# Performance work log

Measured on AMD Instinct MI355X. Metric: run time of the kernel, lower is better.

## Reference

```python
import math
import jax, jax.numpy as jnp
import numpy as np

# Constants (module-level in original repo; plausible biological values)
LATENCY_EPSILON = 1e-6
HAIR_CELL_COMPRESSION_EXPONENT = 0.3
HAIR_CELL_ADAPTATION_SUPPRESSION = 0.5
AUDITORY_NERVE_ADAPTATION_DECAY = 0.9
AUDITORY_NERVE_ADAPTATION_RATE = 0.1

SAMPLE_RATE = 16000
N_FFT = 512
N_FILTERS = 128
OUTPUT_SIZE = 262144
N_TIMESTEPS = 128
SPARSITY = 0.05
F_MIN, F_MAX = 80.0, 7600.0


def build_filterbank() -> np.ndarray:
    """Mel triangular filterbank, faithful to _create_filterbank (integer bin edges)."""
    hz_to_mel = lambda hz: 2595.0 * math.log10(1.0 + hz / 700.0)
    mel_to_hz = lambda mel: 700.0 * (10.0 ** (mel / 2595.0) - 1.0)
    mel_pts = np.linspace(hz_to_mel(F_MIN), hz_to_mel(F_MAX), N_FILTERS + 2)
    hz_pts = np.array([mel_to_hz(m) for m in mel_pts])
    bins = (hz_pts * N_FFT / SAMPLE_RATE).astype(np.int64)  # .long() truncation
    fb = np.zeros((N_FILTERS, N_FFT // 2 + 1), dtype=np.float32)
    for i in range(N_FILTERS):
        l, c, r = bins[i], bins[i + 1], bins[i + 2]
        for j in range(l, c):
            if c > l:
                fb[i, j] = (j - l) / (c - l)
        for j in range(c, r):
            if r > c:
                fb[i, j] = (r - j) / (r - c)
    return fb


def setup_inputs() -> dict:
    key = jax.random.key(0)
    k_audio, k_w = jax.random.split(key)
    audio = jax.random.normal(k_audio, (SAMPLE_RATE,), dtype=jnp.float32)
    filterbank = jnp.asarray(build_filterbank())  # [n_filters, n_fft//2+1]
    W = jax.random.normal(k_w, (OUTPUT_SIZE, N_FILTERS), dtype=jnp.float32) * 0.02
    b = jnp.zeros((OUTPUT_SIZE,), dtype=jnp.float32)
    adaptation_state = jnp.zeros((N_FILTERS,), dtype=jnp.float32)
    return {"audio": audio, "filterbank": filterbank, "W": W, "b": b,
            "adaptation_state": adaptation_state}


def reference(audio, filterbank, W, b, adaptation_state):
    # Basilar membrane: rfft with n=N_FFT (truncates audio to first N_FFT samples)
    spec = jnp.fft.rfft(audio, n=N_FFT)            # [n_fft//2+1] complex
    magnitude = jnp.abs(spec).astype(jnp.float32)   # [257]
    cochlear = filterbank @ magnitude               # [n_filters]
    # Hair cell compression
    hair = jnp.power(cochlear + LATENCY_EPSILON, HAIR_CELL_COMPRESSION_EXPONENT)
    adapted = jax.nn.relu(hair - adaptation_state * HAIR_CELL_ADAPTATION_SUPPRESSION)
    # Output projection (torch Linear: x @ W.T + b)
    activity = W @ adapted + b                      # [output_size]
    # Latency coding: high activity -> early spike (vectorized scatter)
    a_min, a_max = activity.min(), activity.max()
    norm = (activity - a_min) / (a_max - a_min + 1e-6)
    latencies = ((1.0 - norm) * (N_TIMESTEPS - 1)).astype(jnp.int32)  # [output_size]
    fire = norm > SPARSITY                           # [output_size]
    # spikes[t, n] = fire[n] and latencies[n] == t
    spikes = (latencies[None, :] == jnp.arange(N_TIMESTEPS, dtype=jnp.int32)[:, None]) \
             & fire[None, :]                         # [n_timesteps, output_size] bool
    return spikes
```

## Files before the change

kernel.cpp:

```cpp
#include <hip/hip_runtime.h>
#include <math.h>

#ifndef M_PI
#define M_PI 3.14159265358979323846
#endif

#define N_FFT       512
#define N_BINS      257
#define N_FILTERS   128
#define OUTPUT_SIZE 262144
#define N_TIMESTEPS 128

__device__ __forceinline__ unsigned long long enc_d(double f) {
    unsigned long long u = (unsigned long long)__double_as_longlong(f);
    return (u & 0x8000000000000000ull) ? ~u : (u | 0x8000000000000000ull);
}
__device__ __forceinline__ double dec_d(unsigned long long e) {
    unsigned long long u = (e & 0x8000000000000000ull) ? (e ^ 0x8000000000000000ull) : ~e;
    return __longlong_as_double((long long)u);
}

__global__ __launch_bounds__(256) void k1_frontend(
    const float* __restrict__ audio, const float* __restrict__ fb,
    const float* __restrict__ adapt, double* __restrict__ adapted,
    unsigned long long* __restrict__ minmax)
{
    __shared__ double tw_c[N_FFT];
    __shared__ double tw_s[N_FFT];
    __shared__ double aud[N_FFT];
    __shared__ float  mag[N_BINS];

    const int tid = threadIdx.x;

    for (int m = tid; m < N_FFT; m += 256) {
        double ang = (-2.0 * M_PI * (double)m) / (double)N_FFT;
        double s, c;
        sincos(ang, &s, &c);
        tw_c[m] = c;
        tw_s[m] = s;
        aud[m] = (double)audio[m];
    }
    __syncthreads();

    for (int b = tid; b < N_BINS; b += 256) {
        double re = 0.0, im = 0.0;
        int m = 0;
        for (int n = 0; n < N_FFT; ++n) {
            double a = aud[n];
            re += a * tw_c[m];
            im += a * tw_s[m];
            m = (m + b) & (N_FFT - 1);
        }
        mag[b] = (float)sqrt(re * re + im * im);
    }
    __syncthreads();

    if (tid < N_FILTERS) {
        double acc = 0.0;
        const float* row = fb + tid * N_BINS;
        for (int j = 0; j < N_BINS; ++j)
            acc += (double)row[j] * (double)mag[j];
        double x = acc + 1e-6;
        double p = pow(x, 0.3);
        double a = p - (double)adapt[tid] * 0.5;
        adapted[tid] = a > 0.0 ? a : 0.0;
    }
    if (tid == 0) {
        minmax[0] = 0xFFFFFFFFFFFFFFFFull;
        minmax[1] = 0ull;
    }
}

__global__ __launch_bounds__(256) void k2_gemv(
    const float4* __restrict__ W4, const float* __restrict__ bias,
    const double* __restrict__ adapted, double* __restrict__ activity,
    unsigned long long* __restrict__ minmax)
{
    __shared__ double ad[N_FILTERS];
    __shared__ double red_min[256];
    __shared__ double red_max[256];

    const int tid = threadIdx.x;
    if (tid < N_FILTERS) ad[tid] = adapted[tid];
    __syncthreads();

    const int row = blockIdx.x * 256 + tid;
    const float4* wrow = W4 + (size_t)row * (N_FILTERS / 4);

    double acc = 0.0;
    #pragma unroll 8
    for (int j = 0; j < N_FILTERS / 4; ++j) {
        float4 w = wrow[j];
        const int k = j * 4;
        acc += (double)w.x * ad[k];
        acc += (double)w.y * ad[k + 1];
        acc += (double)w.z * ad[k + 2];
        acc += (double)w.w * ad[k + 3];
    }
    double a = acc + (double)bias[row];
    activity[row] = a;

    red_min[tid] = a;
    red_max[tid] = a;
    __syncthreads();
    for (int s = 128; s > 0; s >>= 1) {
        if (tid < s) {
            red_min[tid] = fmin(red_min[tid], red_min[tid + s]);
            red_max[tid] = fmax(red_max[tid], red_max[tid + s]);
        }
        __syncthreads();
    }
    if (tid == 0) {
        atomicMin(&minmax[0], enc_d(red_min[0]));
        atomicMax(&minmax[1], enc_d(red_max[0]));
    }
}

__global__ __launch_bounds__(256) void k3_spikes(
    const double* __restrict__ activity,
    const unsigned long long* __restrict__ minmax,
    int4* __restrict__ out4)
{
    const int tid = blockIdx.x * 256 + threadIdx.x;
    const double amin = dec_d(minmax[0]);
    const double amax = dec_d(minmax[1]);
    const double denom = (amax - amin) + 1e-6;

    const double ax = activity[4 * tid + 0];
    const double ay = activity[4 * tid + 1];
    const double az = activity[4 * tid + 2];
    const double aw = activity[4 * tid + 3];

    const double nx = (ax - amin) / denom;
    const double ny = (ay - amin) / denom;
    const double nz = (az - amin) / denom;
    const double nw = (aw - amin) / denom;

    const int lx = (int)((1.0 - nx) * 127.0);
    const int ly = (int)((1.0 - ny) * 127.0);
    const int lz = (int)((1.0 - nz) * 127.0);
    const int lw = (int)((1.0 - nw) * 127.0);

    const int vx = (nx > 0.05) ? 1 : 0;
    const int vy = (ny > 0.05) ? 1 : 0;
    const int vz = (nz > 0.05) ? 1 : 0;
    const int vw = (nw > 0.05) ? 1 : 0;

    #pragma unroll 4
    for (int t = 0; t < N_TIMESTEPS; ++t) {
        int4 v;
        v.x = (lx == t) ? vx : 0;
        v.y = (ly == t) ? vy : 0;
        v.z = (lz == t) ? vz : 0;
        v.w = (lw == t) ? vw : 0;
        out4[(size_t)t * (OUTPUT_SIZE / 4) + tid] = v;
    }
}

extern "C" void kernel_launch(void* const* d_in, const int* in_sizes, int n_in,
                              void* d_out, int out_size, void* d_ws, size_t ws_size,
                              hipStream_t stream) {
    (void)in_sizes; (void)n_in; (void)out_size; (void)ws_size;

    const float* audio = (const float*)d_in[0];
    const float* fb    = (const float*)d_in[1];
    const float* W     = (const float*)d_in[2];
    const float* bias  = (const float*)d_in[3];
    const float* adapt = (const float*)d_in[4];
    int* out = (int*)d_out;

    double* activity = (double*)d_ws;
    double* adapted  = activity + OUTPUT_SIZE;
    unsigned long long* minmax =
        (unsigned long long*)(adapted + N_FILTERS);

    k1_frontend<<<1, 256, 0, stream>>>(audio, fb, adapt, adapted, minmax);
    k2_gemv<<<OUTPUT_SIZE / 256, 256, 0, stream>>>(
        (const float4*)W, bias, adapted, activity, minmax);
    k3_spikes<<<(OUTPUT_SIZE / 4) / 256, 256, 0, stream>>>(
        activity, minmax, (int4*)out);
}
```

Measured before the change: 316.6 us.

## Split DFT bins across two half-sums and spread spike stores over timestep grid

The single-block frontend now runs with 512 threads and has each thread compute half of one DFT bin's sum, then combines the two partials through shared memory. This roughly halves the serial DFT latency on that one block. The spike kernel gains a second grid dimension so each block writes only a quarter of the timesteps, with nontemporal vector stores. That gives more blocks in flight for the 128 MB output write, but each block reloads the activity values and recomputes the normalization four times.

Measured after the change: 341.2 us. 1.08x slower.

```diff
diff --git a/kernel.cpp b/kernel.cpp
--- a/kernel.cpp
+++ b/kernel.cpp
@@ -11,6 +11,8 @@
 #define OUTPUT_SIZE 262144
 #define N_TIMESTEPS 128
 
+typedef int int4v __attribute__((ext_vector_type(4)));
+
 __device__ __forceinline__ unsigned long long enc_d(double f) {
     unsigned long long u = (unsigned long long)__double_as_longlong(f);
     return (u & 0x8000000000000000ull) ? ~u : (u | 0x8000000000000000ull);
@@ -20,7 +22,7 @@
     return __longlong_as_double((long long)u);
 }
 
-__global__ __launch_bounds__(256) void k1_frontend(
+__global__ __launch_bounds__(512) void k1_frontend(
     const float* __restrict__ audio, const float* __restrict__ fb,
     const float* __restrict__ adapt, double* __restrict__ adapted,
     unsigned long long* __restrict__ minmax)
@@ -28,41 +30,55 @@
     __shared__ double tw_c[N_FFT];
     __shared__ double tw_s[N_FFT];
     __shared__ double aud[N_FFT];
+    __shared__ double re_p[2 * N_BINS];
+    __shared__ double im_p[2 * N_BINS];
     __shared__ float  mag[N_BINS];
 
     const int tid = threadIdx.x;
 
-    for (int m = tid; m < N_FFT; m += 256) {
-        double ang = (-2.0 * M_PI * (double)m) / (double)N_FFT;
+    if (tid < N_FFT) {
+        double ang = (-2.0 * M_PI * (double)tid) / (double)N_FFT;
         double s, c;
         sincos(ang, &s, &c);
-        tw_c[m] = c;
-        tw_s[m] = s;
-        aud[m] = (double)audio[m];
+        tw_c[tid] = c;
+        tw_s[tid] = s;
+        aud[tid] = (double)audio[tid];
     }
     __syncthreads();
 
-    for (int b = tid; b < N_BINS; b += 256) {
+    for (int w = tid; w < 2 * N_BINS; w += 512) {
+        const int b  = w >> 1;
+        const int n0 = (w & 1) * 256;
         double re = 0.0, im = 0.0;
-        int m = 0;
-        for (int n = 0; n < N_FFT; ++n) {
-            double a = aud[n];
+        #pragma unroll 8
+        for (int j = 0; j < 256; ++j) {
+            const int n = n0 + j;
+            const int m = (b * n) & (N_FFT - 1);
+            const double a = aud[n];
             re += a * tw_c[m];
             im += a * tw_s[m];
-            m = (m + b) & (N_FFT - 1);
         }
-        mag[b] = (float)sqrt(re * re + im * im);
+        re_p[w] = re;
+        im_p[w] = im;
+    }
+    __syncthreads();
+
+    if (tid < N_BINS) {
+        const double re = re_p[2 * tid] + re_p[2 * tid + 1];
+        const double im = im_p[2 * tid] + im_p[2 * tid + 1];
+        mag[tid] = (float)sqrt(re * re + im * im);
     }
     __syncthreads();
 
     if (tid < N_FILTERS) {
         double acc = 0.0;
         const float* row = fb + tid * N_BINS;
+        #pragma unroll 4
         for (int j = 0; j < N_BINS; ++j)
             acc += (double)row[j] * (double)mag[j];
-        double x = acc + 1e-6;
-        double p = pow(x, 0.3);
-        double a = p - (double)adapt[tid] * 0.5;
+        const double x = acc + 1e-6;
+        const double p = pow(x, 0.3);
+        const double a = p - (double)adapt[tid] * 0.5;
         adapted[tid] = a > 0.0 ? a : 0.0;
     }
     if (tid == 0) {
@@ -119,22 +135,17 @@
 __global__ __launch_bounds__(256) void k3_spikes(
     const double* __restrict__ activity,
     const unsigned long long* __restrict__ minmax,
-    int4* __restrict__ out4)
+    int4v* __restrict__ out4)
 {
     const int tid = blockIdx.x * 256 + threadIdx.x;
     const double amin = dec_d(minmax[0]);
     const double amax = dec_d(minmax[1]);
     const double denom = (amax - amin) + 1e-6;
 
-    const double ax = activity[4 * tid + 0];
-    const double ay = activity[4 * tid + 1];
-    const double az = activity[4 * tid + 2];
-    const double aw = activity[4 * tid + 3];
-
-    const double nx = (ax - amin) / denom;
-    const double ny = (ay - amin) / denom;
-    const double nz = (az - amin) / denom;
-    const double nw = (aw - amin) / denom;
+    const double nx = (activity[4 * tid + 0] - amin) / denom;
+    const double ny = (activity[4 * tid + 1] - amin) / denom;
+    const double nz = (activity[4 * tid + 2] - amin) / denom;
+    const double nw = (activity[4 * tid + 3] - amin) / denom;
 
     const int lx = (int)((1.0 - nx) * 127.0);
     const int ly = (int)((1.0 - ny) * 127.0);
@@ -146,14 +157,15 @@
     const int vz = (nz > 0.05) ? 1 : 0;
     const int vw = (nw > 0.05) ? 1 : 0;
 
-    #pragma unroll 4
-    for (int t = 0; t < N_TIMESTEPS; ++t) {
-        int4 v;
+    const int t0 = blockIdx.y * (N_TIMESTEPS / 4);
+    #pragma unroll 8
+    for (int t = t0; t < t0 + N_TIMESTEPS / 4; ++t) {
+        int4v v;
         v.x = (lx == t) ? vx : 0;
         v.y = (ly == t) ? vy : 0;
         v.z = (lz == t) ? vz : 0;
         v.w = (lw == t) ? vw : 0;
-        out4[(size_t)t * (OUTPUT_SIZE / 4) + tid] = v;
+        __builtin_nontemporal_store(v, &out4[(size_t)t * (OUTPUT_SIZE / 4) + tid]);
     }
 }
 
@@ -174,9 +186,9 @@
     unsigned long long* minmax =
         (unsigned long long*)(adapted + N_FILTERS);
 
-    k1_frontend<<<1, 256, 0, stream>>>(audio, fb, adapt, adapted, minmax);
+    k1_frontend<<<1, 512, 0, stream>>>(audio, fb, adapt, adapted, minmax);
     k2_gemv<<<OUTPUT_SIZE / 256, 256, 0, stream>>>(
         (const float4*)W, bias, adapted, activity, minmax);
-    k3_spikes<<<(OUTPUT_SIZE / 4) / 256, 256, 0, stream>>>(
-        activity, minmax, (int4*)out);
+    k3_spikes<<<dim3(OUTPUT_SIZE / 4 / 256, 4), 256, 0, stream>>>(
+        activity, minmax, (int4v*)out);
 }
```
